# Performance work log

Hardware: AMD Instinct MI355X
Metric: run time of the kernel (lower is better)

Reference implementation:

```python
import jax, jax.numpy as jnp
import numpy as np


def setup_inputs() -> dict:
    key = jax.random.key(0)
    ks = jax.random.split(key, 4)
    B, T, C, L, DQ = 8, 2048, 256, 32, 512
    return {
        "vis_feats": jax.random.normal(ks[0], (B, T, C), dtype=jnp.float32),
        "query": jax.random.normal(ks[1], (B, L, DQ), dtype=jnp.float32),
        "W1": jax.random.normal(ks[2], (DQ, C), dtype=jnp.float32) / np.float32(np.sqrt(DQ)),
        "b1": jnp.zeros((C,), dtype=jnp.float32),
        "W2": jax.random.normal(ks[3], (DQ, C), dtype=jnp.float32) / np.float32(np.sqrt(DQ)),
        "b2": jnp.zeros((C,), dtype=jnp.float32),
        "window_size": 32,
        "num_chunks": 8,
    }


def reference(vis_feats, query, W1, b1, W2, b2, window_size, num_chunks):
    B, T, C = vis_feats.shape
    L = query.shape[1]
    # seq encoders (modeled as linear projections): [B, L, C]
    enc1 = query @ W1 + b1
    enc2 = query @ W2 + b2
    # clip-word similarity and per-clip word label: [B, T]
    sim = jnp.einsum("btc,blc->btl", vis_feats, enc1)
    clip_labels = jnp.argmax(sim, axis=2)
    NW = T - window_size + 1
    cic = window_size // num_chunks  # clips per chunk
    # sliding-window unfold indices: [NW, window_size]
    idx = jnp.arange(NW)[:, None] + jnp.arange(window_size)[None, :]
    vis_unf = vis_feats[:, idx, :]                      # [B, NW, W, C]
    lab_unf = clip_labels[:, idx].reshape(B, NW, num_chunks, cic)
    # majority vote per chunk == argmax of label histogram (ties -> smallest label,
    # matching np.bincount + np.argmax)
    counts = jax.nn.one_hot(lab_unf, L, dtype=jnp.int32).sum(axis=3)  # [B, NW, K, L]
    lbls = jnp.argmax(counts, axis=-1)                  # [B, NW, K]
    # adaptive_avg_pool3d (K, cic, C) -> (K, 1, C) == mean over clips-in-chunk
    pooled = vis_unf.reshape(B, NW, num_chunks, cic, C).mean(axis=3)  # [B, NW, K, C]
    # gather the majority-vote word encoding and modulate
    gathered = enc2[jnp.arange(B)[:, None, None], lbls]  # [B, NW, K, C]
    return gathered * pooled
```

## Files before the change

### kernel.cpp

```cpp
#include <hip/hip_runtime.h>
#include <hip/hip_bf16.h>

#define B   8
#define T   2048
#define C   256
#define L   32
#define DQ  512
#define NW  2017
#define NK  8
#define CIC 4
#define WT  32
#define SROWS (WT + (NK-1)*CIC)
#define LT  32

typedef float nfloat4 __attribute__((ext_vector_type(4)));

__global__ __launch_bounds__(256) void enc_kernel(
    const float* __restrict__ query, const float* __restrict__ W1,
    const float* __restrict__ b1, const float* __restrict__ W2,
    const float* __restrict__ b2, float* __restrict__ enc1,
    float* __restrict__ enc2) {
  const int lg = blockIdx.x, b = blockIdx.y, cs = blockIdx.z;
  const int tid = threadIdx.x;
  const int tx = tid & 63;
  const int dq = tid >> 6;
  const int c = cs * 64 + tx;
  __shared__ float4 qs4[4][DQ / 4];
  __shared__ float red[2][4][4][64];

  const float4* q4 = (const float4*)(query + ((size_t)b * L + lg * 4) * DQ);
  for (int i = tid; i < 4 * (DQ / 4); i += 256) {
    const int j = i >> 7, g = i & 127;
    qs4[j][g] = q4[j * (DQ / 4) + g];
  }
  __syncthreads();

  float a1[4] = {0.f, 0.f, 0.f, 0.f};
  float a2[4] = {0.f, 0.f, 0.f, 0.f};
  const int g0 = dq * 32;
#pragma unroll 4
  for (int gg = 0; gg < 32; ++gg) {
    const int g = g0 + gg;
    const float4 q0 = qs4[0][g], q1 = qs4[1][g], q2 = qs4[2][g], q3 = qs4[3][g];
    const float* wp1 = W1 + (size_t)(4 * g) * C + c;
    const float* wp2 = W2 + (size_t)(4 * g) * C + c;
    const float w10 = wp1[0], w11 = wp1[C], w12 = wp1[2 * C], w13 = wp1[3 * C];
    const float w20 = wp2[0], w21 = wp2[C], w22 = wp2[2 * C], w23 = wp2[3 * C];
    a1[0] = fmaf(q0.x, w10, fmaf(q0.y, w11, fmaf(q0.z, w12, fmaf(q0.w, w13, a1[0]))));
    a1[1] = fmaf(q1.x, w10, fmaf(q1.y, w11, fmaf(q1.z, w12, fmaf(q1.w, w13, a1[1]))));
    a1[2] = fmaf(q2.x, w10, fmaf(q2.y, w11, fmaf(q2.z, w12, fmaf(q2.w, w13, a1[2]))));
    a1[3] = fmaf(q3.x, w10, fmaf(q3.y, w11, fmaf(q3.z, w12, fmaf(q3.w, w13, a1[3]))));
    a2[0] = fmaf(q0.x, w20, fmaf(q0.y, w21, fmaf(q0.z, w22, fmaf(q0.w, w23, a2[0]))));
    a2[1] = fmaf(q1.x, w20, fmaf(q1.y, w21, fmaf(q1.z, w22, fmaf(q1.w, w23, a2[1]))));
    a2[2] = fmaf(q2.x, w20, fmaf(q2.y, w21, fmaf(q2.z, w22, fmaf(q2.w, w23, a2[2]))));
    a2[3] = fmaf(q3.x, w20, fmaf(q3.y, w21, fmaf(q3.z, w22, fmaf(q3.w, w23, a2[3]))));
  }
#pragma unroll
  for (int j = 0; j < 4; ++j) {
    red[0][dq][j][tx] = a1[j];
    red[1][dq][j][tx] = a2[j];
  }
  __syncthreads();

  for (int o = tid; o < 512; o += 256) {
    const int e = o >> 8, j = (o >> 6) & 3, t = o & 63;
    const float v = red[e][0][j][t] + red[e][1][j][t] +
                    red[e][2][j][t] + red[e][3][j][t];
    const int cc = cs * 64 + t;
    const size_t off = ((size_t)b * L + lg * 4 + j) * C + cc;
    if (e == 0) enc1[off] = v + b1[cc];
    else        enc2[off] = v + b2[cc];
  }
}

__global__ __launch_bounds__(256) void label_kernel(
    const float* __restrict__ vis, const float* __restrict__ enc1,
    int* __restrict__ labels) {
  const int b = blockIdx.y;
  const int t0 = blockIdx.x * LT;
  const int tid = threadIdx.x;
  const int l = tid & 31;
  const int part = tid >> 5;
  __shared__ float4 raw[LT * (C / 4)];
  __shared__ alignas(16) float pacc[4][LT][36];

  float4 ef[8];
  {
    const float4* e1p = (const float4*)(enc1 + ((size_t)b * L + l) * C) + part * 8;
#pragma unroll
    for (int j = 0; j < 8; ++j) ef[j] = e1p[j];
  }
  const float4* vb = (const float4*)(vis + (size_t)b * T * C);
  for (int i = tid; i < LT * (C / 4); i += 256)
    raw[i] = vb[(size_t)(t0 + (i >> 6)) * (C / 4) + (i & 63)];
  __syncthreads();

  for (int t = 0; t < LT; ++t) {
    const float4* vr = &raw[t * (C / 4) + part * 8];
    float a = 0.f;
#pragma unroll
    for (int j = 0; j < 8; ++j) {
      const float4 v = vr[j];
      a = fmaf(v.x, ef[j].x, fmaf(v.y, ef[j].y, fmaf(v.z, ef[j].z, fmaf(v.w, ef[j].w, a))));
    }
    a += __shfl_down(a, 32);
    if (!(tid & 32)) pacc[tid >> 6][t][l] = a;
  }
  __syncthreads();

  if (tid < LT) {
    float4 s4[8];
#pragma unroll
    for (int j = 0; j < 8; ++j) s4[j] = make_float4(0.f, 0.f, 0.f, 0.f);
#pragma unroll
    for (int p = 0; p < 4; ++p) {
      const float4* pp = (const float4*)pacc[p][tid];
#pragma unroll
      for (int j = 0; j < 8; ++j) {
        s4[j].x += pp[j].x; s4[j].y += pp[j].y;
        s4[j].z += pp[j].z; s4[j].w += pp[j].w;
      }
    }
    float bv = -INFINITY;
    int bi = 0;
#pragma unroll
    for (int j = 0; j < 8; ++j) {
      if (s4[j].x > bv) { bv = s4[j].x; bi = 4 * j; }
      if (s4[j].y > bv) { bv = s4[j].y; bi = 4 * j + 1; }
      if (s4[j].z > bv) { bv = s4[j].z; bi = 4 * j + 2; }
      if (s4[j].w > bv) { bv = s4[j].w; bi = 4 * j + 3; }
    }
    labels[(size_t)b * T + t0 + tid] = bi;
  }
}

__global__ __launch_bounds__(256) void out_kernel(
    const float* __restrict__ vis, const float* __restrict__ enc2,
    const int* __restrict__ labels, float* __restrict__ out) {
  const int b = blockIdx.y;
  const int w0 = blockIdx.x * WT;
  const int tid = threadIdx.x;
  const int lane = tid & 63;
  const int wv = tid >> 6;
  __shared__ float4 S4[SROWS * (C / 4)];
  __shared__ int slbl[SROWS];

  int l0 = 0, l1 = 0, l2 = 0, l3 = 0;
  if (tid < SROWS) {
    const int* lb = labels + (size_t)b * T;
    const int t = w0 + tid;
#define LCL(tt) lb[(tt) > (T - 1) ? (T - 1) : (tt)]
    l0 = LCL(t); l1 = LCL(t + 1); l2 = LCL(t + 2); l3 = LCL(t + 3);
#undef LCL
  }

  const float4* vb = (const float4*)(vis + (size_t)b * T * C);
  float4 r[18];
  {
    const int s0 = wv * (SROWS / 4);
#pragma unroll
    for (int j = 0; j < 18; ++j) {
      int t = w0 + s0 + j;
      t = t > (T - 1) ? (T - 1) : t;
      r[j] = vb[(size_t)t * (C / 4) + lane];
    }
  }

  if (tid < SROWS) {
    const int c0 = 1 + (l0 == l1) + (l0 == l2) + (l0 == l3);
    const int c1 = 1 + (l1 == l0) + (l1 == l2) + (l1 == l3);
    const int c2 = 1 + (l2 == l0) + (l2 == l1) + (l2 == l3);
    const int c3 = 1 + (l3 == l0) + (l3 == l1) + (l3 == l2);
    int best = l0, bc = c0;
    if (c1 > bc || (c1 == bc && l1 < best)) { best = l1; bc = c1; }
    if (c2 > bc || (c2 == bc && l2 < best)) { best = l2; bc = c2; }
    if (c3 > bc || (c3 == bc && l3 < best)) { best = l3; bc = c3; }
    slbl[tid] = best;
  }

  {
    const int s0 = wv * (SROWS / 4);
#pragma unroll
    for (int s = 0; s < SROWS / 4; ++s) {
      float4 o;
      o.x = (r[s].x + r[s + 1].x + r[s + 2].x + r[s + 3].x) * 0.25f;
      o.y = (r[s].y + r[s + 1].y + r[s + 2].y + r[s + 3].y) * 0.25f;
      o.z = (r[s].z + r[s + 1].z + r[s + 2].z + r[s + 3].z) * 0.25f;
      o.w = (r[s].w + r[s + 1].w + r[s + 2].w + r[s + 3].w) * 0.25f;
      S4[(s0 + s) * (C / 4) + lane] = o;
    }
  }
  __syncthreads();

  const float4* e2b = (const float4*)(enc2 + (size_t)b * L * C);
  nfloat4* outp = (nfloat4*)out;
  const int wlim = (NW - w0) < WT ? (NW - w0) : WT;
#pragma unroll
  for (int kk = 0; kk < 2; ++kk) {
    const int k = wv + kk * 4;
#pragma unroll 4
    for (int w = 0; w < wlim; ++w) {
      const int s = w + CIC * k;
      const int lb = slbl[s];
      const float4 e = e2b[lb * (C / 4) + lane];
      const float4 sv = S4[s * (C / 4) + lane];
      nfloat4 o;
      o.x = e.x * sv.x; o.y = e.y * sv.y; o.z = e.z * sv.z; o.w = e.w * sv.w;
      __builtin_nontemporal_store(
          o, &outp[(((size_t)b * NW + w0 + w) * NK + k) * (C / 4) + lane]);
    }
  }
}

extern "C" void kernel_launch(void* const* d_in, const int* in_sizes, int n_in,
                              void* d_out, int out_size, void* d_ws, size_t ws_size,
                              hipStream_t stream) {
  const float* vis   = (const float*)d_in[0];
  const float* query = (const float*)d_in[1];
  const float* W1    = (const float*)d_in[2];
  const float* b1    = (const float*)d_in[3];
  const float* W2    = (const float*)d_in[4];
  const float* b2    = (const float*)d_in[5];
  float* out = (float*)d_out;

  float* enc1 = (float*)d_ws;
  float* enc2 = enc1 + (size_t)B * L * C;
  int* labels = (int*)(enc2 + (size_t)B * L * C);

  enc_kernel<<<dim3(8, B, 4), 256, 0, stream>>>(query, W1, b1, W2, b2, enc1, enc2);
  label_kernel<<<dim3(T / LT, B), 256, 0, stream>>>(vis, enc1, labels);
  out_kernel<<<dim3((NW + WT - 1) / WT, B), 256, 0, stream>>>(vis, enc2, labels, out);
}
```

Baseline: 186.3 us.

## Fuse label computation into output kernel, recomputing halo labels per block

Merges the label and output kernels into one kernel. Each block computes clip labels for its window span plus a halo of 31 rows, in two shared-memory chunks, then runs the majority vote and pooling directly from shared memory. This removes one kernel launch and the global round-trip of the label array. In exchange it recomputes about twice as many similarity dot products because the halos overlap, and shared-memory use grows to about 69KB per block, which may lower occupancy.

```diff
diff --git a/kernel.cpp b/kernel.cpp
--- a/kernel.cpp
+++ b/kernel.cpp
@@ -11,7 +11,7 @@
 #define CIC 4
 #define WT  32
 #define SROWS (WT + (NK-1)*CIC)
-#define LT  32
+#define LROWS (SROWS + 3)
 
 typedef float nfloat4 __attribute__((ext_vector_type(4)));
 
@@ -73,16 +73,23 @@
   }
 }
 
-__global__ __launch_bounds__(256) void label_kernel(
+__global__ __launch_bounds__(256) void fused_kernel(
     const float* __restrict__ vis, const float* __restrict__ enc1,
-    int* __restrict__ labels) {
+    const float* __restrict__ enc2, float* __restrict__ out) {
   const int b = blockIdx.y;
-  const int t0 = blockIdx.x * LT;
+  const int w0 = blockIdx.x * WT;
   const int tid = threadIdx.x;
+  const int lane = tid & 63;
+  const int wv = tid >> 6;
   const int l = tid & 31;
   const int part = tid >> 5;
-  __shared__ float4 raw[LT * (C / 4)];
-  __shared__ alignas(16) float pacc[4][LT][36];
+
+  __shared__ alignas(16) char smem[69056];
+  float4* raw = (float4*)smem;
+  float (*pacc)[LROWS][36] = (float (*)[LROWS][36])(smem + 32768);
+  float4* S4 = (float4*)smem;
+  __shared__ int lbl[LROWS];
+  __shared__ int slbl[SROWS];
 
   float4 ef[8];
   {
@@ -91,24 +98,33 @@
     for (int j = 0; j < 8; ++j) ef[j] = e1p[j];
   }
   const float4* vb = (const float4*)(vis + (size_t)b * T * C);
-  for (int i = tid; i < LT * (C / 4); i += 256)
-    raw[i] = vb[(size_t)(t0 + (i >> 6)) * (C / 4) + (i & 63)];
-  __syncthreads();
-
-  for (int t = 0; t < LT; ++t) {
-    const float4* vr = &raw[t * (C / 4) + part * 8];
-    float a = 0.f;
-#pragma unroll
-    for (int j = 0; j < 8; ++j) {
-      const float4 v = vr[j];
-      a = fmaf(v.x, ef[j].x, fmaf(v.y, ef[j].y, fmaf(v.z, ef[j].z, fmaf(v.w, ef[j].w, a))));
-    }
-    a += __shfl_down(a, 32);
-    if (!(tid & 32)) pacc[tid >> 6][t][l] = a;
-  }
-  __syncthreads();
-
-  if (tid < LT) {
+
+#pragma unroll 1
+  for (int ch = 0; ch < 2; ++ch) {
+    const int base = ch * 32;
+    const int nrows = ch ? (LROWS - 32) : 32;
+    if (ch) __syncthreads();
+    for (int i = tid; i < nrows * 64; i += 256) {
+      int t = w0 + base + (i >> 6);
+      t = t > (T - 1) ? (T - 1) : t;
+      raw[i] = vb[(size_t)t * 64 + (i & 63)];
+    }
+    __syncthreads();
+    for (int t = 0; t < nrows; ++t) {
+      const float4* vr = &raw[t * 64 + part * 8];
+      float a = 0.f;
+#pragma unroll
+      for (int j = 0; j < 8; ++j) {
+        const float4 v = vr[j];
+        a = fmaf(v.x, ef[j].x, fmaf(v.y, ef[j].y, fmaf(v.z, ef[j].z, fmaf(v.w, ef[j].w, a))));
+      }
+      a += __shfl_down(a, 32);
+      if (!(tid & 32)) pacc[tid >> 6][base + t][l] = a;
+    }
+  }
+  __syncthreads();
+
+  if (tid < LROWS) {
     float4 s4[8];
 #pragma unroll
     for (int j = 0; j < 8; ++j) s4[j] = make_float4(0.f, 0.f, 0.f, 0.f);
@@ -130,31 +146,10 @@
       if (s4[j].z > bv) { bv = s4[j].z; bi = 4 * j + 2; }
       if (s4[j].w > bv) { bv = s4[j].w; bi = 4 * j + 3; }
     }
-    labels[(size_t)b * T + t0 + tid] = bi;
-  }
-}
-
-__global__ __launch_bounds__(256) void out_kernel(
-    const float* __restrict__ vis, const float* __restrict__ enc2,
-    const int* __restrict__ labels, float* __restrict__ out) {
-  const int b = blockIdx.y;
-  const int w0 = blockIdx.x * WT;
-  const int tid = threadIdx.x;
-  const int lane = tid & 63;
-  const int wv = tid >> 6;
-  __shared__ float4 S4[SROWS * (C / 4)];
-  __shared__ int slbl[SROWS];
-
-  int l0 = 0, l1 = 0, l2 = 0, l3 = 0;
-  if (tid < SROWS) {
-    const int* lb = labels + (size_t)b * T;
-    const int t = w0 + tid;
-#define LCL(tt) lb[(tt) > (T - 1) ? (T - 1) : (tt)]
-    l0 = LCL(t); l1 = LCL(t + 1); l2 = LCL(t + 2); l3 = LCL(t + 3);
-#undef LCL
-  }
-
-  const float4* vb = (const float4*)(vis + (size_t)b * T * C);
+    lbl[tid] = bi;
+  }
+  __syncthreads();
+
   float4 r[18];
   {
     const int s0 = wv * (SROWS / 4);
@@ -162,11 +157,12 @@
     for (int j = 0; j < 18; ++j) {
       int t = w0 + s0 + j;
       t = t > (T - 1) ? (T - 1) : t;
-      r[j] = vb[(size_t)t * (C / 4) + lane];
+      r[j] = vb[(size_t)t * 64 + lane];
     }
   }
 
   if (tid < SROWS) {
+    const int l0 = lbl[tid], l1 = lbl[tid + 1], l2 = lbl[tid + 2], l3 = lbl[tid + 3];
     const int c0 = 1 + (l0 == l1) + (l0 == l2) + (l0 == l3);
     const int c1 = 1 + (l1 == l0) + (l1 == l2) + (l1 == l3);
     const int c2 = 1 + (l2 == l0) + (l2 == l1) + (l2 == l3);
@@ -187,7 +183,7 @@
       o.y = (r[s].y + r[s + 1].y + r[s + 2].y + r[s + 3].y) * 0.25f;
       o.z = (r[s].z + r[s + 1].z + r[s + 2].z + r[s + 3].z) * 0.25f;
       o.w = (r[s].w + r[s + 1].w + r[s + 2].w + r[s + 3].w) * 0.25f;
-      S4[(s0 + s) * (C / 4) + lane] = o;
+      S4[(s0 + s) * 64 + lane] = o;
     }
   }
   __syncthreads();
@@ -202,12 +198,12 @@
     for (int w = 0; w < wlim; ++w) {
       const int s = w + CIC * k;
       const int lb = slbl[s];
-      const float4 e = e2b[lb * (C / 4) + lane];
-      const float4 sv = S4[s * (C / 4) + lane];
+      const float4 e = e2b[lb * 64 + lane];
+      const float4 sv = S4[s * 64 + lane];
       nfloat4 o;
       o.x = e.x * sv.x; o.y = e.y * sv.y; o.z = e.z * sv.z; o.w = e.w * sv.w;
       __builtin_nontemporal_store(
-          o, &outp[(((size_t)b * NW + w0 + w) * NK + k) * (C / 4) + lane]);
+          o, &outp[(((size_t)b * NW + w0 + w) * NK + k) * 64 + lane]);
     }
   }
 }
@@ -225,9 +221,7 @@
 
   float* enc1 = (float*)d_ws;
   float* enc2 = enc1 + (size_t)B * L * C;
-  int* labels = (int*)(enc2 + (size_t)B * L * C);
 
   enc_kernel<<<dim3(8, B, 4), 256, 0, stream>>>(query, W1, b1, W2, b2, enc1, enc2);
-  label_kernel<<<dim3(T / LT, B), 256, 0, stream>>>(vis, enc1, labels);
-  out_kernel<<<dim3((NW + WT - 1) / WT, B), 256, 0, stream>>>(vis, enc2, labels, out);
+  fused_kernel<<<dim3((NW + WT - 1) / WT, B), 256, 0, stream>>>(vis, enc1, enc2, out);
 }
```

Measured after the change: 191.2 us. 2.6% more time.

## Restructure label kernel to register-tiled dot products with shuffle argmax

Applied to the files above, without the earlier changes.

Rewrites the clip-word similarity kernel so each thread computes four word scores for one clip row. Both vis rows and enc1 are staged in shared memory, with padding and a rotation swizzle to avoid bank conflicts. The shared-memory partial-sum buffer and the single-warp final reduction are replaced by a warp-shuffle argmax across 8 lanes. The summation order changes, which could flip argmax ties in rare cases.

```diff
diff --git a/kernel.cpp b/kernel.cpp
--- a/kernel.cpp
+++ b/kernel.cpp
@@ -79,59 +79,71 @@
   const int b = blockIdx.y;
   const int t0 = blockIdx.x * LT;
   const int tid = threadIdx.x;
-  const int l = tid & 31;
-  const int part = tid >> 5;
-  __shared__ float4 raw[LT * (C / 4)];
-  __shared__ alignas(16) float pacc[4][LT][36];
-
-  float4 ef[8];
-  {
-    const float4* e1p = (const float4*)(enc1 + ((size_t)b * L + l) * C) + part * 8;
-#pragma unroll
-    for (int j = 0; j < 8; ++j) ef[j] = e1p[j];
-  }
+  const int lg = tid & 7;
+  const int row = tid >> 3;
+
+  __shared__ float4 vis_s[32 * 65];
+  __shared__ float4 e1_s[32 * 64];
+
   const float4* vb = (const float4*)(vis + (size_t)b * T * C);
-  for (int i = tid; i < LT * (C / 4); i += 256)
-    raw[i] = vb[(size_t)(t0 + (i >> 6)) * (C / 4) + (i & 63)];
-  __syncthreads();
-
-  for (int t = 0; t < LT; ++t) {
-    const float4* vr = &raw[t * (C / 4) + part * 8];
-    float a = 0.f;
-#pragma unroll
-    for (int j = 0; j < 8; ++j) {
-      const float4 v = vr[j];
-      a = fmaf(v.x, ef[j].x, fmaf(v.y, ef[j].y, fmaf(v.z, ef[j].z, fmaf(v.w, ef[j].w, a))));
-    }
-    a += __shfl_down(a, 32);
-    if (!(tid & 32)) pacc[tid >> 6][t][l] = a;
-  }
-  __syncthreads();
-
-  if (tid < LT) {
-    float4 s4[8];
-#pragma unroll
-    for (int j = 0; j < 8; ++j) s4[j] = make_float4(0.f, 0.f, 0.f, 0.f);
-#pragma unroll
-    for (int p = 0; p < 4; ++p) {
-      const float4* pp = (const float4*)pacc[p][tid];
+  for (int i = tid; i < 32 * 64; i += 256) {
+    const int r = i >> 6, c4 = i & 63;
+    vis_s[r * 65 + c4] = vb[(size_t)(t0 + r) * 64 + c4];
+  }
+  const float4* e1g = (const float4*)(enc1 + (size_t)b * L * C);
+  for (int i = tid; i < 32 * 64; i += 256) {
+    const int l = i >> 6, c4 = i & 63;
+    e1_s[l * 64 + ((c4 + l) & 63)] = e1g[l * 64 + c4];
+  }
+  __syncthreads();
+
+  float run[4], cur[4];
+#pragma unroll
+  for (int cp = 0; cp < 4; ++cp) {
+#pragma unroll
+    for (int e = 0; e < 2; ++e) {
+      const int g = cp * 2 + e;
+      float a[4] = {0.f, 0.f, 0.f, 0.f};
 #pragma unroll
       for (int j = 0; j < 8; ++j) {
-        s4[j].x += pp[j].x; s4[j].y += pp[j].y;
-        s4[j].z += pp[j].z; s4[j].w += pp[j].w;
+        const float4 v = vis_s[row * 65 + g * 8 + j];
+#pragma unroll
+        for (int q = 0; q < 4; ++q) {
+          const int l = lg + 8 * q;
+          const float4 ev = e1_s[l * 64 + ((g * 8 + j + l) & 63)];
+          a[q] = fmaf(v.x, ev.x,
+                 fmaf(v.y, ev.y,
+                 fmaf(v.z, ev.z,
+                 fmaf(v.w, ev.w, a[q]))));
+        }
       }
-    }
-    float bv = -INFINITY;
-    int bi = 0;
-#pragma unroll
-    for (int j = 0; j < 8; ++j) {
-      if (s4[j].x > bv) { bv = s4[j].x; bi = 4 * j; }
-      if (s4[j].y > bv) { bv = s4[j].y; bi = 4 * j + 1; }
-      if (s4[j].z > bv) { bv = s4[j].z; bi = 4 * j + 2; }
-      if (s4[j].w > bv) { bv = s4[j].w; bi = 4 * j + 3; }
-    }
-    labels[(size_t)b * T + t0 + tid] = bi;
-  }
+      if (e == 0) {
+#pragma unroll
+        for (int q = 0; q < 4; ++q) cur[q] = a[q];
+      } else {
+#pragma unroll
+        for (int q = 0; q < 4; ++q) {
+          const float pair = cur[q] + a[q];
+          run[q] = cp ? (run[q] + pair) : pair;
+        }
+      }
+    }
+  }
+
+  float bv = run[0];
+  int bl = lg;
+#pragma unroll
+  for (int q = 1; q < 4; ++q) {
+    const int l = lg + 8 * q;
+    if (run[q] > bv) { bv = run[q]; bl = l; }
+  }
+#pragma unroll
+  for (int m = 1; m < 8; m <<= 1) {
+    const float ov = __shfl_xor(bv, m, 64);
+    const int ol = __shfl_xor(bl, m, 64);
+    if (ov > bv || (ov == bv && ol < bl)) { bv = ov; bl = ol; }
+  }
+  if (lg == 0) labels[(size_t)b * T + t0 + row] = bl;
 }
 
 __global__ __launch_bounds__(256) void out_kernel(
```

New measurement: 191.7 us. 2.9% more time.

## Split output kernel into single-wave blocks per chunk without shared memory

Applied to the files above, without the earlier changes.

The output kernel now launches one 64-thread wave per (batch, 16-window tile, chunk) instead of 256-thread blocks covering 32 windows and all chunks. Each wave loads its own 19 rows and labels into registers and computes pooling and the majority vote inline, which drops shared memory and the block barrier. The aim is more independent blocks and latency hiding on the store-bound output write. The cost is redundant reads of vis and labels across chunks and tiles, plus redundant vote computation per chunk.

```diff
diff --git a/kernel.cpp b/kernel.cpp
--- a/kernel.cpp
+++ b/kernel.cpp
@@ -9,9 +9,9 @@
 #define NW  2017
 #define NK  8
 #define CIC 4
-#define WT  32
-#define SROWS (WT + (NK-1)*CIC)
 #define LT  32
+#define OWT 16
+#define NTILE 1016
 
 typedef float nfloat4 __attribute__((ext_vector_type(4)));
 
@@ -134,80 +134,62 @@
   }
 }
 
-__global__ __launch_bounds__(256) void out_kernel(
+__global__ __launch_bounds__(64) void out_kernel(
     const float* __restrict__ vis, const float* __restrict__ enc2,
     const int* __restrict__ labels, float* __restrict__ out) {
-  const int b = blockIdx.y;
-  const int w0 = blockIdx.x * WT;
-  const int tid = threadIdx.x;
-  const int lane = tid & 63;
-  const int wv = tid >> 6;
-  __shared__ float4 S4[SROWS * (C / 4)];
-  __shared__ int slbl[SROWS];
-
-  int l0 = 0, l1 = 0, l2 = 0, l3 = 0;
-  if (tid < SROWS) {
-    const int* lb = labels + (size_t)b * T;
-    const int t = w0 + tid;
-#define LCL(tt) lb[(tt) > (T - 1) ? (T - 1) : (tt)]
-    l0 = LCL(t); l1 = LCL(t + 1); l2 = LCL(t + 2); l3 = LCL(t + 3);
-#undef LCL
-  }
+  const int bid = blockIdx.x;
+  const int tile = bid % NTILE;
+  const int k = bid / NTILE;
+  const int b = tile / 127;
+  const int w0 = (tile % 127) * OWT;
+  const int lane = threadIdx.x;
+  const int base = w0 + CIC * k;
 
   const float4* vb = (const float4*)(vis + (size_t)b * T * C);
-  float4 r[18];
-  {
-    const int s0 = wv * (SROWS / 4);
-#pragma unroll
-    for (int j = 0; j < 18; ++j) {
-      int t = w0 + s0 + j;
-      t = t > (T - 1) ? (T - 1) : t;
-      r[j] = vb[(size_t)t * (C / 4) + lane];
-    }
-  }
-
-  if (tid < SROWS) {
-    const int c0 = 1 + (l0 == l1) + (l0 == l2) + (l0 == l3);
-    const int c1 = 1 + (l1 == l0) + (l1 == l2) + (l1 == l3);
-    const int c2 = 1 + (l2 == l0) + (l2 == l1) + (l2 == l3);
-    const int c3 = 1 + (l3 == l0) + (l3 == l1) + (l3 == l2);
-    int best = l0, bc = c0;
-    if (c1 > bc || (c1 == bc && l1 < best)) { best = l1; bc = c1; }
-    if (c2 > bc || (c2 == bc && l2 < best)) { best = l2; bc = c2; }
-    if (c3 > bc || (c3 == bc && l3 < best)) { best = l3; bc = c3; }
-    slbl[tid] = best;
-  }
-
-  {
-    const int s0 = wv * (SROWS / 4);
-#pragma unroll
-    for (int s = 0; s < SROWS / 4; ++s) {
-      float4 o;
-      o.x = (r[s].x + r[s + 1].x + r[s + 2].x + r[s + 3].x) * 0.25f;
-      o.y = (r[s].y + r[s + 1].y + r[s + 2].y + r[s + 3].y) * 0.25f;
-      o.z = (r[s].z + r[s + 1].z + r[s + 2].z + r[s + 3].z) * 0.25f;
-      o.w = (r[s].w + r[s + 1].w + r[s + 2].w + r[s + 3].w) * 0.25f;
-      S4[(s0 + s) * (C / 4) + lane] = o;
-    }
-  }
-  __syncthreads();
+  float4 r[OWT + 3];
+#pragma unroll
+  for (int j = 0; j < OWT + 3; ++j) {
+    int t = base + j;
+    t = t > (T - 1) ? (T - 1) : t;
+    r[j] = vb[(size_t)t * (C / 4) + lane];
+  }
+
+  const int* lb = labels + (size_t)b * T;
+  int la[OWT + 3];
+#pragma unroll
+  for (int j = 0; j < OWT + 3; ++j) {
+    int t = base + j;
+    t = t > (T - 1) ? (T - 1) : t;
+    la[j] = lb[t];
+  }
 
   const float4* e2b = (const float4*)(enc2 + (size_t)b * L * C);
   nfloat4* outp = (nfloat4*)out;
-  const int wlim = (NW - w0) < WT ? (NW - w0) : WT;
-#pragma unroll
-  for (int kk = 0; kk < 2; ++kk) {
-    const int k = wv + kk * 4;
-#pragma unroll 4
-    for (int w = 0; w < wlim; ++w) {
-      const int s = w + CIC * k;
-      const int lb = slbl[s];
-      const float4 e = e2b[lb * (C / 4) + lane];
-      const float4 sv = S4[s * (C / 4) + lane];
+  const int wlim = (NW - w0) < OWT ? (NW - w0) : OWT;
+  const size_t obase = (((size_t)b * NW + w0) * NK + k) * (C / 4) + lane;
+
+#pragma unroll
+  for (int w = 0; w < OWT; ++w) {
+    if (w < wlim) {
+      const int l0 = la[w], l1 = la[w + 1], l2 = la[w + 2], l3 = la[w + 3];
+      const int c0 = 1 + (l0 == l1) + (l0 == l2) + (l0 == l3);
+      const int c1 = 1 + (l1 == l0) + (l1 == l2) + (l1 == l3);
+      const int c2 = 1 + (l2 == l0) + (l2 == l1) + (l2 == l3);
+      const int c3 = 1 + (l3 == l0) + (l3 == l1) + (l3 == l2);
+      int best = l0, bc = c0;
+      if (c1 > bc || (c1 == bc && l1 < best)) { best = l1; bc = c1; }
+      if (c2 > bc || (c2 == bc && l2 < best)) { best = l2; bc = c2; }
+      if (c3 > bc || (c3 == bc && l3 < best)) { best = l3; bc = c3; }
+
+      const float4 e = e2b[best * (C / 4) + lane];
+      float4 p;
+      p.x = (r[w].x + r[w + 1].x + r[w + 2].x + r[w + 3].x) * 0.25f;
+      p.y = (r[w].y + r[w + 1].y + r[w + 2].y + r[w + 3].y) * 0.25f;
+      p.z = (r[w].z + r[w + 1].z + r[w + 2].z + r[w + 3].z) * 0.25f;
+      p.w = (r[w].w + r[w + 1].w + r[w + 2].w + r[w + 3].w) * 0.25f;
       nfloat4 o;
-      o.x = e.x * sv.x; o.y = e.y * sv.y; o.z = e.z * sv.z; o.w = e.w * sv.w;
-      __builtin_nontemporal_store(
-          o, &outp[(((size_t)b * NW + w0 + w) * NK + k) * (C / 4) + lane]);
+      o.x = e.x * p.x; o.y = e.y * p.y; o.z = e.z * p.z; o.w = e.w * p.w;
+      __builtin_nontemporal_store(o, &outp[obase + (size_t)w * NK * (C / 4)]);
     }
   }
 }
@@ -229,5 +211,5 @@
 
   enc_kernel<<<dim3(8, B, 4), 256, 0, stream>>>(query, W1, b1, W2, b2, enc1, enc2);
   label_kernel<<<dim3(T / LT, B), 256, 0, stream>>>(vis, enc1, labels);
-  out_kernel<<<dim3((NW + WT - 1) / WT, B), 256, 0, stream>>>(vis, enc2, labels, out);
-}
+  out_kernel<<<dim3(NTILE * NK), 64, 0, stream>>>(vis, enc2, labels, out);
+}
```

Measured after the change: 190.6 us. 1.02x slower.
